# Kernel tuning notes

Measured on AMD Instinct MI355X. Metric: run time of the kernel, lower is better.

Reference implementation:

```python
import jax, jax.numpy as jnp
import numpy as np

# NVFP4 e2m1 representable magnitudes and nearest-rounding decision boundaries
FP4_GRID = jnp.array([0.0, 0.5, 1.0, 1.5, 2.0, 3.0, 4.0, 6.0], dtype=jnp.float32)
FP4_BOUNDS = jnp.array([0.25, 0.75, 1.25, 1.75, 2.5, 3.5, 5.0], dtype=jnp.float32)
E4M3_MAX = 448.0
FP4_MAX = 6.0
BLOCK = 16  # NVFP4 block size along K


def round_fp4(x):
    """Round to nearest FP4 (e2m1) representable value (saturating at +-6)."""
    idx = jnp.searchsorted(FP4_BOUNDS, jnp.abs(x))
    return jnp.sign(x) * FP4_GRID[idx]


def cast_e4m3(x):
    """Saturating cast through float8_e4m3fn and back to fp32."""
    return jnp.clip(x, -E4M3_MAX, E4M3_MAX).astype(jnp.float8_e4m3fn).astype(jnp.float32)


def setup_inputs() -> dict:
    key = jax.random.key(0)
    kx, kw, kb = jax.random.split(key, 3)
    M, N, K = 32, 8192, 8192
    x = jax.random.normal(kx, (M, K), dtype=jnp.float32)
    w = jax.random.normal(kw, (N, K), dtype=jnp.float32)
    bias = jax.random.normal(kb, (N,), dtype=jnp.float32)

    # raw global scales: amax / (448 * 6)  (== 1 / fp4_global_scale)
    weight_scale_2 = jnp.max(jnp.abs(w)) / (E4M3_MAX * FP4_MAX)
    input_scale = jnp.max(jnp.abs(x)) / (E4M3_MAX * FP4_MAX)

    # offline NVFP4 quantization of the weight (as done in __init__)
    wb = w.reshape(N, K // BLOCK, BLOCK)
    sf = jnp.max(jnp.abs(wb), axis=-1) / FP4_MAX              # [N, K//16] per-block scale
    weight_scale = cast_e4m3(sf / weight_scale_2)             # fp8 block scales (values)
    dscale = weight_scale[..., None] * weight_scale_2         # per-element dequant scale
    safe = jnp.where(dscale > 0, dscale, 1.0)
    w_fp4 = jnp.where(dscale > 0, round_fp4(wb / safe), 0.0).reshape(N, K)

    return {
        "x": x,
        "weight_fp4": w_fp4,
        "bias": bias,
        "input_scale": input_scale.reshape(1),
        "weight_scale": weight_scale,
        "weight_scale_2": weight_scale_2.reshape(1),
    }


def reference(x, weight_fp4, bias, input_scale, weight_scale, weight_scale_2):
    N, K = weight_fp4.shape
    M = x.shape[0]
    # --- weight dequant: fp4 value * fp8 block scale * global scale ---
    w_dq = (weight_fp4.reshape(N, K // BLOCK, BLOCK)
            * weight_scale[..., None] * weight_scale_2).reshape(N, K)
    # --- dynamic NVFP4 fake-quant of the activation ---
    xb = x.reshape(M, K // BLOCK, BLOCK)
    sf = cast_e4m3(jnp.max(jnp.abs(xb), axis=-1) / FP4_MAX / input_scale)  # [M, K//16]
    scale = sf[..., None] * input_scale                                    # per-element scale
    safe = jnp.where(scale > 0, scale, 1.0)
    x_dq = jnp.where(scale > 0, round_fp4(xb / safe) * scale, 0.0).reshape(M, K)
    # --- linear ---
    return x_dq @ w_dq.T + bias
```

## Files before the change

### kernel.cpp

```cpp
#include <hip/hip_runtime.h>

typedef float f32x4 __attribute__((ext_vector_type(4)));
typedef short s16x8 __attribute__((ext_vector_type(8)));

#define M_DIM 32
#define N_DIM 8192
#define K_DIM 8192
#define NBLK (K_DIM / 16)
#define KSPLIT 4
#define WSTEPS 16
#define SCL_LD 129

__device__ inline unsigned short f2bf(float f) {
    unsigned int u = __float_as_uint(f);
    u = (u + 0x7FFFu + ((u >> 16) & 1u)) >> 16;
    return (unsigned short)u;
}

__device__ inline float round_fp4(float x) {
    float a = fabsf(x);
    float g;
    if (a > 2.5f)        g = (a > 5.0f) ? 6.0f : ((a > 3.5f) ? 4.0f : 3.0f);
    else if (a > 1.25f)  g = (a > 1.75f) ? 2.0f : 1.5f;
    else                 g = (a > 0.75f) ? 1.0f : ((a > 0.25f) ? 0.5f : 0.0f);
    return copysignf(g, x);
}

__device__ inline float cast_e4m3(float v) {
    v = fminf(v, 448.0f);
    if (v < 0.015625f) {
        return rintf(v * 512.0f) * (1.0f / 512.0f);
    }
    int e; float m = frexpf(v, &e);
    return ldexpf(rintf(m * 16.0f) * 0.0625f, e);
}

__global__ void prep_kernel(const float* __restrict__ x,
                            const float* __restrict__ input_scale,
                            const float* __restrict__ bias,
                            unsigned short* __restrict__ xpack,
                            float* __restrict__ out) {
    if (blockIdx.x >= 64) {
        int i = (blockIdx.x - 64) * blockDim.x + threadIdx.x;
        f32x4 b = *(const f32x4*)(bias + ((i * 4) & (N_DIM - 1)));
        *(f32x4*)(out + (size_t)i * 4) = b;
        return;
    }
    int tid = blockIdx.x * blockDim.x + threadIdx.x;
    int m = tid >> 9;
    int b = tid & 511;
    const float is = input_scale[0];

    const float* xp = x + (size_t)m * K_DIM + b * 16;
    f32x4 l0 = *(const f32x4*)(xp);
    f32x4 l1 = *(const f32x4*)(xp + 4);
    f32x4 l2 = *(const f32x4*)(xp + 8);
    f32x4 l3 = *(const f32x4*)(xp + 12);
    float v[16];
    #pragma unroll
    for (int i = 0; i < 4; ++i) { v[i]=l0[i]; v[4+i]=l1[i]; v[8+i]=l2[i]; v[12+i]=l3[i]; }

    float amax = 0.f;
    #pragma unroll
    for (int i = 0; i < 16; ++i) amax = fmaxf(amax, fabsf(v[i]));

    float sf = cast_e4m3(amax / 6.0f / is);
    float scale = sf * is;

    int kstep = b >> 1;
    int t = m >> 4;
    int mrow = m & 15;
    unsigned short* base = xpack + (size_t)kstep * 1024 + t * 512;
    #pragma unroll
    for (int i = 0; i < 16; ++i) {
        float q = 0.f;
        if (scale > 0.f) q = round_fp4(v[i] / scale) * scale;
        int g = ((b & 1) << 1) + (i >> 3);
        int lane = g * 16 + mrow;
        int j = i & 7;
        base[lane * 8 + j] = f2bf(q);
    }
}

__global__ __launch_bounds__(256, 8) void gemm_kernel(
    const float* __restrict__ W,
    const float* __restrict__ wscale,
    const float* __restrict__ ws2p,
    const unsigned short* __restrict__ xpack,
    float* __restrict__ out)
{
    __shared__ float shm[16 * SCL_LD];

    const int bid   = blockIdx.x;
    const int xcd   = bid & 7;
    const int local = bid >> 3;
    const int ntile = xcd * 64 + (local >> 2);
    const int kb    = local & 3;

    const int wave = threadIdx.x >> 6;
    const int lane = threadIdx.x & 63;
    const int lrow = lane & 15;
    const int lgrp = lane >> 4;
    const int n0 = ntile * 16;
    const float ws2 = ws2p[0];

    {
        int t = threadIdx.x;
        int row = t >> 4;
        int c0 = (t & 15) * 8;
        const float* s = wscale + (size_t)(n0 + row) * NBLK + kb * 128 + c0;
        #pragma unroll
        for (int j = 0; j < 8; ++j)
            shm[row * SCL_LD + c0 + j] = s[j] * ws2;
    }
    __syncthreads();

    const int kofs = kb * 2048 + wave * 512;
    const float* wcur = W + (size_t)(n0 + lrow) * K_DIM + kofs + lgrp * 8;
    const unsigned short* xcur = xpack + (size_t)(kofs >> 5) * 1024 + lane * 8;
    const float* sbase = shm + lrow * SCL_LD + wave * 32 + (lgrp >> 1);

    f32x4 acc0 = {0,0,0,0}, acc1 = {0,0,0,0};

    f32x4 a0 = *(const f32x4*)(wcur);
    f32x4 a1 = *(const f32x4*)(wcur + 4);
    s16x8 b0 = *(const s16x8*)(xcur);
    s16x8 b1 = *(const s16x8*)(xcur + 512);

    #pragma unroll
    for (int s = 0; s < WSTEPS; ++s) {
        f32x4 na0, na1; s16x8 nb0, nb1;
        if (s + 1 < WSTEPS) {
            na0 = *(const f32x4*)(wcur + 32);
            na1 = *(const f32x4*)(wcur + 36);
            nb0 = *(const s16x8*)(xcur + 1024);
            nb1 = *(const s16x8*)(xcur + 1536);
        }
        float sc = sbase[s * 2];
        s16x8 af;
        #pragma unroll
        for (int j = 0; j < 4; ++j) {
            af[j]     = (short)f2bf(a0[j] * sc);
            af[4 + j] = (short)f2bf(a1[j] * sc);
        }
        acc0 = __builtin_amdgcn_mfma_f32_16x16x32_bf16(af, b0, acc0, 0, 0, 0);
        acc1 = __builtin_amdgcn_mfma_f32_16x16x32_bf16(af, b1, acc1, 0, 0, 0);
        a0 = na0; a1 = na1; b0 = nb0; b1 = nb1;
        wcur += 32;
        xcur += 1024;
    }

    __syncthreads();
    float* red = shm;
    #pragma unroll
    for (int r = 0; r < 4; ++r) {
        red[wave * 512 + lane * 8 + r]     = acc0[r];
        red[wave * 512 + lane * 8 + 4 + r] = acc1[r];
    }
    __syncthreads();

    #pragma unroll
    for (int h = 0; h < 2; ++h) {
        int j = threadIdx.x + h * 256;
        float v = red[j] + red[512 + j] + red[1024 + j] + red[1536 + j];
        int l = j >> 3, t = (j >> 2) & 1, r = j & 3;
        int m = t * 16 + (l & 15);
        int n = n0 + ((l >> 4) << 2) + r;
        atomicAdd(out + (size_t)m * N_DIM + n, v);
    }
}

extern "C" void kernel_launch(void* const* d_in, const int* in_sizes, int n_in,
                              void* d_out, int out_size, void* d_ws, size_t ws_size,
                              hipStream_t stream) {
    const float* x           = (const float*)d_in[0];
    const float* weight_fp4  = (const float*)d_in[1];
    const float* bias        = (const float*)d_in[2];
    const float* input_scale = (const float*)d_in[3];
    const float* wscale      = (const float*)d_in[4];
    const float* ws2         = (const float*)d_in[5];
    float* out = (float*)d_out;
    unsigned short* xpack = (unsigned short*)d_ws;

    prep_kernel<<<320, 256, 0, stream>>>(x, input_scale, bias, xpack, out);
    gemm_kernel<<<2048, 256, 0, stream>>>(weight_fp4, wscale, ws2, xpack, out);
}
```

Measured before the change: 67.22 us.

## Switch GEMM to 32x32x16 MFMA with 32-row N tiles and 8-way K split

Replaces the pair of 16x16x32 bf16 MFMAs per step with two 32x32x16 MFMAs. Each block now covers 32 weight rows and all 32 activation rows, and K is split 8 ways instead of 4, keeping the block count at 2048. The activation pack layout in the prep kernel is changed to match, with vectorized stores. The aim is to issue fewer MFMA and load instructions per FLOP and to reuse each weight row across the full M dimension. In exchange the kernel does more shared-memory reduction work and more atomics per output element because of the deeper K split.

```diff
diff --git a/kernel.cpp b/kernel.cpp
--- a/kernel.cpp
+++ b/kernel.cpp
@@ -1,15 +1,16 @@
 #include <hip/hip_runtime.h>
 
 typedef float f32x4 __attribute__((ext_vector_type(4)));
-typedef short s16x8 __attribute__((ext_vector_type(8)));
+typedef short s16x4 __attribute__((ext_vector_type(4)));
+typedef float f32x16 __attribute__((ext_vector_type(16)));
 
 #define M_DIM 32
 #define N_DIM 8192
 #define K_DIM 8192
 #define NBLK (K_DIM / 16)
-#define KSPLIT 4
-#define WSTEPS 16
-#define SCL_LD 129
+#define KSPLIT 8
+#define SSTEPS 8
+#define SCL_LD 66
 
 __device__ inline unsigned short f2bf(float f) {
     unsigned int u = __float_as_uint(f);
@@ -67,18 +68,21 @@
     float sf = cast_e4m3(amax / 6.0f / is);
     float scale = sf * is;
 
-    int kstep = b >> 1;
-    int t = m >> 4;
-    int mrow = m & 15;
-    unsigned short* base = xpack + (size_t)kstep * 1024 + t * 512;
-    #pragma unroll
-    for (int i = 0; i < 16; ++i) {
-        float q = 0.f;
-        if (scale > 0.f) q = round_fp4(v[i] / scale) * scale;
-        int g = ((b & 1) << 1) + (i >> 3);
-        int lane = g * 16 + mrow;
-        int j = i & 7;
-        base[lane * 8 + j] = f2bf(q);
+    int ss = b >> 1;
+    int t  = b & 1;
+    unsigned short* base = xpack + ((size_t)ss * 4 + t * 2) * 256 + m * 8;
+    #pragma unroll
+    for (int h = 0; h < 2; ++h) {
+        unsigned short tmp[8];
+        #pragma unroll
+        for (int j = 0; j < 8; ++j) {
+            float q = 0.f;
+            int i = h * 8 + j;
+            if (scale > 0.f) q = round_fp4(v[i] / scale) * scale;
+            tmp[j] = f2bf(q);
+        }
+        *(s16x4*)(base + h * 256)     = *(s16x4*)(tmp);
+        *(s16x4*)(base + h * 256 + 4) = *(s16x4*)(tmp + 4);
     }
 }
 
@@ -89,63 +93,84 @@
     const unsigned short* __restrict__ xpack,
     float* __restrict__ out)
 {
-    __shared__ float shm[16 * SCL_LD];
+    __shared__ float shm[4096];
 
     const int bid   = blockIdx.x;
     const int xcd   = bid & 7;
     const int local = bid >> 3;
-    const int ntile = xcd * 64 + (local >> 2);
-    const int kb    = local & 3;
+    const int ntile = xcd * 32 + (local >> 3);
+    const int kb    = local & 7;
 
     const int wave = threadIdx.x >> 6;
     const int lane = threadIdx.x & 63;
-    const int lrow = lane & 15;
-    const int lgrp = lane >> 4;
-    const int n0 = ntile * 16;
+    const int lrow = lane & 31;
+    const int half = lane >> 5;
+    const int n0 = ntile * 32;
     const float ws2 = ws2p[0];
 
     {
         int t = threadIdx.x;
-        int row = t >> 4;
-        int c0 = (t & 15) * 8;
-        const float* s = wscale + (size_t)(n0 + row) * NBLK + kb * 128 + c0;
+        int row = t >> 3;
+        int c0 = (t & 7) * 8;
+        const float* s = wscale + (size_t)(n0 + row) * NBLK + kb * 64 + c0;
         #pragma unroll
         for (int j = 0; j < 8; ++j)
             shm[row * SCL_LD + c0 + j] = s[j] * ws2;
     }
     __syncthreads();
 
-    const int kofs = kb * 2048 + wave * 512;
-    const float* wcur = W + (size_t)(n0 + lrow) * K_DIM + kofs + lgrp * 8;
-    const unsigned short* xcur = xpack + (size_t)(kofs >> 5) * 1024 + lane * 8;
-    const float* sbase = shm + lrow * SCL_LD + wave * 32 + (lgrp >> 1);
-
-    f32x4 acc0 = {0,0,0,0}, acc1 = {0,0,0,0};
-
-    f32x4 a0 = *(const f32x4*)(wcur);
-    f32x4 a1 = *(const f32x4*)(wcur + 4);
-    s16x8 b0 = *(const s16x8*)(xcur);
-    s16x8 b1 = *(const s16x8*)(xcur + 512);
-
-    #pragma unroll
-    for (int s = 0; s < WSTEPS; ++s) {
-        f32x4 na0, na1; s16x8 nb0, nb1;
-        if (s + 1 < WSTEPS) {
-            na0 = *(const f32x4*)(wcur + 32);
-            na1 = *(const f32x4*)(wcur + 36);
-            nb0 = *(const s16x8*)(xcur + 1024);
-            nb1 = *(const s16x8*)(xcur + 1536);
-        }
-        float sc = sbase[s * 2];
-        s16x8 af;
+    const int kofs = kb * 1024 + wave * 256;
+    const float* wcur = W + (size_t)(n0 + lrow) * K_DIM + kofs + half * 8;
+    const unsigned short* xcur = xpack + ((size_t)(kofs >> 5) * 4 + half) * 256 + lrow * 8;
+    const float* sbase = shm + lrow * SCL_LD + (kofs >> 4) - (size_t)(n0 + 0) * 0 - kb * 64 + 0;
+    const float* scur = shm + lrow * SCL_LD + wave * 16;
+
+    f32x16 acc = {};
+
+    f32x4 a00 = *(const f32x4*)(wcur);
+    f32x4 a01 = *(const f32x4*)(wcur + 4);
+    f32x4 a10 = *(const f32x4*)(wcur + 16);
+    f32x4 a11 = *(const f32x4*)(wcur + 20);
+    s16x4 b00 = *(const s16x4*)(xcur);
+    s16x4 b01 = *(const s16x4*)(xcur + 4);
+    s16x4 b10 = *(const s16x4*)(xcur + 512);
+    s16x4 b11 = *(const s16x4*)(xcur + 516);
+
+    #pragma unroll
+    for (int s = 0; s < SSTEPS; ++s) {
+        f32x4 na00, na01, na10, na11; s16x4 nb00, nb01, nb10, nb11;
+        if (s + 1 < SSTEPS) {
+            na00 = *(const f32x4*)(wcur + 32);
+            na01 = *(const f32x4*)(wcur + 36);
+            na10 = *(const f32x4*)(wcur + 48);
+            na11 = *(const f32x4*)(wcur + 52);
+            nb00 = *(const s16x4*)(xcur + 1024);
+            nb01 = *(const s16x4*)(xcur + 1028);
+            nb10 = *(const s16x4*)(xcur + 1536);
+            nb11 = *(const s16x4*)(xcur + 1540);
+        }
+        float sc0 = scur[2 * s];
+        float sc1 = scur[2 * s + 1];
+        typedef short s16x8 __attribute__((ext_vector_type(8)));
+        s16x8 af, bf;
         #pragma unroll
         for (int j = 0; j < 4; ++j) {
-            af[j]     = (short)f2bf(a0[j] * sc);
-            af[4 + j] = (short)f2bf(a1[j] * sc);
-        }
-        acc0 = __builtin_amdgcn_mfma_f32_16x16x32_bf16(af, b0, acc0, 0, 0, 0);
-        acc1 = __builtin_amdgcn_mfma_f32_16x16x32_bf16(af, b1, acc1, 0, 0, 0);
-        a0 = na0; a1 = na1; b0 = nb0; b1 = nb1;
+            af[j]     = (short)f2bf(a00[j] * sc0);
+            af[4 + j] = (short)f2bf(a01[j] * sc0);
+            bf[j]     = b00[j];
+            bf[4 + j] = b01[j];
+        }
+        acc = __builtin_amdgcn_mfma_f32_32x32x16_bf16(af, bf, acc, 0, 0, 0);
+        #pragma unroll
+        for (int j = 0; j < 4; ++j) {
+            af[j]     = (short)f2bf(a10[j] * sc1);
+            af[4 + j] = (short)f2bf(a11[j] * sc1);
+            bf[j]     = b10[j];
+            bf[4 + j] = b11[j];
+        }
+        acc = __builtin_amdgcn_mfma_f32_32x32x16_bf16(af, bf, acc, 0, 0, 0);
+        a00 = na00; a01 = na01; a10 = na10; a11 = na11;
+        b00 = nb00; b01 = nb01; b10 = nb10; b11 = nb11;
         wcur += 32;
         xcur += 1024;
     }
@@ -153,19 +178,18 @@
     __syncthreads();
     float* red = shm;
     #pragma unroll
-    for (int r = 0; r < 4; ++r) {
-        red[wave * 512 + lane * 8 + r]     = acc0[r];
-        red[wave * 512 + lane * 8 + 4 + r] = acc1[r];
+    for (int r = 0; r < 16; ++r) {
+        int row = (r & 3) + 8 * (r >> 2) + 4 * half;
+        red[wave * 1024 + row * 32 + lrow] = acc[r];
     }
     __syncthreads();
 
     #pragma unroll
-    for (int h = 0; h < 2; ++h) {
+    for (int h = 0; h < 4; ++h) {
         int j = threadIdx.x + h * 256;
-        float v = red[j] + red[512 + j] + red[1024 + j] + red[1536 + j];
-        int l = j >> 3, t = (j >> 2) & 1, r = j & 3;
-        int m = t * 16 + (l & 15);
-        int n = n0 + ((l >> 4) << 2) + r;
+        float v = red[j] + red[1024 + j] + red[2048 + j] + red[3072 + j];
+        int m = j & 31;
+        int n = n0 + (j >> 5);
         atomicAdd(out + (size_t)m * N_DIM + n, v);
     }
 }
```

Result: slower. 93.41 us (+39.0%).

## Widen GEMM tiles to 32 rows of N with 8-way K split

Applied to the files above, without the earlier changes.

Each block now covers 32 weight rows instead of 16 and splits K eight ways instead of four, so each wave issues four MFMAs per step and reuses every activation fragment for two weight row groups. The explicit software prefetch of the next step's loads is removed in favour of issuing all loads at the top of each unrolled step. The reduction layout is changed so the atomic adds go to consecutive m indices. The grid size stays 2048 blocks, so more atomics per output element are traded for better reuse of the activation loads and more memory requests in flight per wave.

```diff
diff --git a/kernel.cpp b/kernel.cpp
--- a/kernel.cpp
+++ b/kernel.cpp
@@ -7,9 +7,8 @@
 #define N_DIM 8192
 #define K_DIM 8192
 #define NBLK (K_DIM / 16)
-#define KSPLIT 4
-#define WSTEPS 16
-#define SCL_LD 129
+#define SSTEPS 8
+#define SCL_LD 65
 
 __device__ inline unsigned short f2bf(float f) {
     unsigned int u = __float_as_uint(f);
@@ -89,83 +88,84 @@
     const unsigned short* __restrict__ xpack,
     float* __restrict__ out)
 {
-    __shared__ float shm[16 * SCL_LD];
+    __shared__ float shm[4096];
 
     const int bid   = blockIdx.x;
     const int xcd   = bid & 7;
     const int local = bid >> 3;
-    const int ntile = xcd * 64 + (local >> 2);
-    const int kb    = local & 3;
+    const int ntile = xcd * 32 + (local >> 3);
+    const int kb    = local & 7;
 
     const int wave = threadIdx.x >> 6;
     const int lane = threadIdx.x & 63;
     const int lrow = lane & 15;
     const int lgrp = lane >> 4;
-    const int n0 = ntile * 16;
+    const int n0 = ntile * 32;
     const float ws2 = ws2p[0];
 
     {
         int t = threadIdx.x;
-        int row = t >> 4;
-        int c0 = (t & 15) * 8;
-        const float* s = wscale + (size_t)(n0 + row) * NBLK + kb * 128 + c0;
+        int row = t >> 3;
+        int c0 = (t & 7) * 8;
+        const float* s = wscale + (size_t)(n0 + row) * NBLK + kb * 64 + c0;
         #pragma unroll
         for (int j = 0; j < 8; ++j)
             shm[row * SCL_LD + c0 + j] = s[j] * ws2;
     }
     __syncthreads();
 
-    const int kofs = kb * 2048 + wave * 512;
-    const float* wcur = W + (size_t)(n0 + lrow) * K_DIM + kofs + lgrp * 8;
+    const int kofs = kb * 1024 + wave * 256;
+    const float* wcur0 = W + (size_t)(n0 + lrow) * K_DIM + kofs + lgrp * 8;
+    const float* wcur1 = wcur0 + (size_t)16 * K_DIM;
     const unsigned short* xcur = xpack + (size_t)(kofs >> 5) * 1024 + lane * 8;
-    const float* sbase = shm + lrow * SCL_LD + wave * 32 + (lgrp >> 1);
+    const float* scur0 = shm + lrow * SCL_LD + wave * 16 + (lgrp >> 1);
+    const float* scur1 = scur0 + 16 * SCL_LD;
 
-    f32x4 acc0 = {0,0,0,0}, acc1 = {0,0,0,0};
-
-    f32x4 a0 = *(const f32x4*)(wcur);
-    f32x4 a1 = *(const f32x4*)(wcur + 4);
-    s16x8 b0 = *(const s16x8*)(xcur);
-    s16x8 b1 = *(const s16x8*)(xcur + 512);
+    f32x4 acc00 = {0,0,0,0}, acc01 = {0,0,0,0};
+    f32x4 acc10 = {0,0,0,0}, acc11 = {0,0,0,0};
 
     #pragma unroll
-    for (int s = 0; s < WSTEPS; ++s) {
-        f32x4 na0, na1; s16x8 nb0, nb1;
-        if (s + 1 < WSTEPS) {
-            na0 = *(const f32x4*)(wcur + 32);
-            na1 = *(const f32x4*)(wcur + 36);
-            nb0 = *(const s16x8*)(xcur + 1024);
-            nb1 = *(const s16x8*)(xcur + 1536);
-        }
-        float sc = sbase[s * 2];
-        s16x8 af;
+    for (int s = 0; s < SSTEPS; ++s) {
+        f32x4 a00 = *(const f32x4*)(wcur0 + s * 32);
+        f32x4 a01 = *(const f32x4*)(wcur0 + s * 32 + 4);
+        f32x4 a10 = *(const f32x4*)(wcur1 + s * 32);
+        f32x4 a11 = *(const f32x4*)(wcur1 + s * 32 + 4);
+        s16x8 b0 = *(const s16x8*)(xcur + (size_t)s * 1024);
+        s16x8 b1 = *(const s16x8*)(xcur + (size_t)s * 1024 + 512);
+        float sc0 = scur0[2 * s];
+        float sc1 = scur1[2 * s];
+        s16x8 af0, af1;
         #pragma unroll
         for (int j = 0; j < 4; ++j) {
-            af[j]     = (short)f2bf(a0[j] * sc);
-            af[4 + j] = (short)f2bf(a1[j] * sc);
+            af0[j]     = (short)f2bf(a00[j] * sc0);
+            af0[4 + j] = (short)f2bf(a01[j] * sc0);
+            af1[j]     = (short)f2bf(a10[j] * sc1);
+            af1[4 + j] = (short)f2bf(a11[j] * sc1);
         }
-        acc0 = __builtin_amdgcn_mfma_f32_16x16x32_bf16(af, b0, acc0, 0, 0, 0);
-        acc1 = __builtin_amdgcn_mfma_f32_16x16x32_bf16(af, b1, acc1, 0, 0, 0);
-        a0 = na0; a1 = na1; b0 = nb0; b1 = nb1;
-        wcur += 32;
-        xcur += 1024;
+        acc00 = __builtin_amdgcn_mfma_f32_16x16x32_bf16(af0, b0, acc00, 0, 0, 0);
+        acc01 = __builtin_amdgcn_mfma_f32_16x16x32_bf16(af0, b1, acc01, 0, 0, 0);
+        acc10 = __builtin_amdgcn_mfma_f32_16x16x32_bf16(af1, b0, acc10, 0, 0, 0);
+        acc11 = __builtin_amdgcn_mfma_f32_16x16x32_bf16(af1, b1, acc11, 0, 0, 0);
     }
 
     __syncthreads();
     float* red = shm;
     #pragma unroll
     for (int r = 0; r < 4; ++r) {
-        red[wave * 512 + lane * 8 + r]     = acc0[r];
-        red[wave * 512 + lane * 8 + 4 + r] = acc1[r];
+        int nl = lgrp * 4 + r;
+        red[wave * 1024 + nl * 32 + lrow]              = acc00[r];
+        red[wave * 1024 + nl * 32 + 16 + lrow]         = acc01[r];
+        red[wave * 1024 + (16 + nl) * 32 + lrow]       = acc10[r];
+        red[wave * 1024 + (16 + nl) * 32 + 16 + lrow]  = acc11[r];
     }
     __syncthreads();
 
     #pragma unroll
-    for (int h = 0; h < 2; ++h) {
+    for (int h = 0; h < 4; ++h) {
         int j = threadIdx.x + h * 256;
-        float v = red[j] + red[512 + j] + red[1024 + j] + red[1536 + j];
-        int l = j >> 3, t = (j >> 2) & 1, r = j & 3;
-        int m = t * 16 + (l & 15);
-        int n = n0 + ((l >> 4) << 2) + r;
+        float v = red[j] + red[1024 + j] + red[2048 + j] + red[3072 + j];
+        int m = j & 31;
+        int n = n0 + (j >> 5);
         atomicAdd(out + (size_t)m * N_DIM + n, v);
     }
 }
```

After: 89.14 us. +32.6%, slower.

## Share activation tile across four N-waves via async LDS load, split K 32-way

Applied to the files above, without the earlier changes.

Each block now covers 64 output columns (one 16-column slice per wave) over a 256-wide K chunk, split 32 ways along K. The packed activation tile for that chunk is staged once into LDS with global_load_lds and reused by all four waves, instead of every wave reading activations from global memory. Per-wave results go straight out through atomics, which removes the cross-wave LDS reduction. The cost is twice as many blocks and far more atomicAdd traffic to the output (a 32-way K split instead of 4), along with shorter per-block loops that have less prefetch depth.

```diff
diff --git a/kernel.cpp b/kernel.cpp
--- a/kernel.cpp
+++ b/kernel.cpp
@@ -7,9 +7,7 @@
 #define N_DIM 8192
 #define K_DIM 8192
 #define NBLK (K_DIM / 16)
-#define KSPLIT 4
-#define WSTEPS 16
-#define SCL_LD 129
+#define SSTEPS 8
 
 __device__ inline unsigned short f2bf(float f) {
     unsigned int u = __float_as_uint(f);
@@ -33,6 +31,11 @@
     }
     int e; float m = frexpf(v, &e);
     return ldexpf(rintf(m * 16.0f) * 0.0625f, e);
+}
+
+__device__ __forceinline__ void async_copy16(const void* g, void* l) {
+    __builtin_amdgcn_global_load_lds((const __attribute__((address_space(1))) void*)g,
+                                     (__attribute__((address_space(3))) void*)l, 16, 0, 0);
 }
 
 __global__ void prep_kernel(const float* __restrict__ x,
@@ -89,54 +92,59 @@
     const unsigned short* __restrict__ xpack,
     float* __restrict__ out)
 {
-    __shared__ float shm[16 * SCL_LD];
+    __shared__ __align__(16) unsigned char xq[16384];
+    __shared__ float sc_lds[1024];
 
     const int bid   = blockIdx.x;
     const int xcd   = bid & 7;
     const int local = bid >> 3;
-    const int ntile = xcd * 64 + (local >> 2);
-    const int kb    = local & 3;
+    const int ntile = xcd * 16 + (local >> 5);
+    const int kb    = local & 31;
 
     const int wave = threadIdx.x >> 6;
     const int lane = threadIdx.x & 63;
     const int lrow = lane & 15;
     const int lgrp = lane >> 4;
-    const int n0 = ntile * 16;
+    const int n0 = ntile * 64;
     const float ws2 = ws2p[0];
 
     {
+        const unsigned short* xsrc = xpack + (size_t)kb * 8192;
+        #pragma unroll
+        for (int i = 0; i < 4; ++i) {
+            int c = i * 4 + wave;
+            async_copy16(xsrc + c * 512 + lane * 8, xq + c * 1024);
+        }
+    }
+    {
         int t = threadIdx.x;
-        int row = t >> 4;
-        int c0 = (t & 15) * 8;
-        const float* s = wscale + (size_t)(n0 + row) * NBLK + kb * 128 + c0;
+        int row = t >> 2;
+        int c0 = (t & 3) * 4;
+        f32x4 s4 = *(const f32x4*)(wscale + (size_t)(n0 + row) * NBLK + kb * 16 + c0);
         #pragma unroll
-        for (int j = 0; j < 8; ++j)
-            shm[row * SCL_LD + c0 + j] = s[j] * ws2;
+        for (int j = 0; j < 4; ++j) s4[j] *= ws2;
+        *(f32x4*)(sc_lds + row * 16 + c0) = s4;
     }
     __syncthreads();
 
-    const int kofs = kb * 2048 + wave * 512;
-    const float* wcur = W + (size_t)(n0 + lrow) * K_DIM + kofs + lgrp * 8;
-    const unsigned short* xcur = xpack + (size_t)(kofs >> 5) * 1024 + lane * 8;
-    const float* sbase = shm + lrow * SCL_LD + wave * 32 + (lgrp >> 1);
+    const float* wcur = W + (size_t)(n0 + wave * 16 + lrow) * K_DIM + kb * 256 + lgrp * 8;
+    const float* scur = sc_lds + (wave * 16 + lrow) * 16 + (lgrp >> 1);
 
     f32x4 acc0 = {0,0,0,0}, acc1 = {0,0,0,0};
 
     f32x4 a0 = *(const f32x4*)(wcur);
     f32x4 a1 = *(const f32x4*)(wcur + 4);
-    s16x8 b0 = *(const s16x8*)(xcur);
-    s16x8 b1 = *(const s16x8*)(xcur + 512);
 
     #pragma unroll
-    for (int s = 0; s < WSTEPS; ++s) {
-        f32x4 na0, na1; s16x8 nb0, nb1;
-        if (s + 1 < WSTEPS) {
+    for (int s = 0; s < SSTEPS; ++s) {
+        f32x4 na0, na1;
+        if (s + 1 < SSTEPS) {
             na0 = *(const f32x4*)(wcur + 32);
             na1 = *(const f32x4*)(wcur + 36);
-            nb0 = *(const s16x8*)(xcur + 1024);
-            nb1 = *(const s16x8*)(xcur + 1536);
         }
-        float sc = sbase[s * 2];
+        s16x8 b0 = *(const s16x8*)(xq + s * 2048 + lane * 16);
+        s16x8 b1 = *(const s16x8*)(xq + s * 2048 + 1024 + lane * 16);
+        float sc = scur[2 * s];
         s16x8 af;
         #pragma unroll
         for (int j = 0; j < 4; ++j) {
@@ -145,28 +153,15 @@
         }
         acc0 = __builtin_amdgcn_mfma_f32_16x16x32_bf16(af, b0, acc0, 0, 0, 0);
         acc1 = __builtin_amdgcn_mfma_f32_16x16x32_bf16(af, b1, acc1, 0, 0, 0);
-        a0 = na0; a1 = na1; b0 = nb0; b1 = nb1;
+        a0 = na0; a1 = na1;
         wcur += 32;
-        xcur += 1024;
     }
 
-    __syncthreads();
-    float* red = shm;
     #pragma unroll
     for (int r = 0; r < 4; ++r) {
-        red[wave * 512 + lane * 8 + r]     = acc0[r];
-        red[wave * 512 + lane * 8 + 4 + r] = acc1[r];
-    }
-    __syncthreads();
-
-    #pragma unroll
-    for (int h = 0; h < 2; ++h) {
-        int j = threadIdx.x + h * 256;
-        float v = red[j] + red[512 + j] + red[1024 + j] + red[1536 + j];
-        int l = j >> 3, t = (j >> 2) & 1, r = j & 3;
-        int m = t * 16 + (l & 15);
-        int n = n0 + ((l >> 4) << 2) + r;
-        atomicAdd(out + (size_t)m * N_DIM + n, v);
+        int n = n0 + wave * 16 + lgrp * 4 + r;
+        atomicAdd(out + (size_t)lrow * N_DIM + n,        acc0[r]);
+        atomicAdd(out + (size_t)(16 + lrow) * N_DIM + n, acc1[r]);
     }
 }
 
@@ -183,5 +178,5 @@
     unsigned short* xpack = (unsigned short*)d_ws;
 
     prep_kernel<<<320, 256, 0, stream>>>(x, input_scale, bias, xpack, out);
-    gemm_kernel<<<2048, 256, 0, stream>>>(weight_fp4, wscale, ws2, xpack, out);
+    gemm_kernel<<<4096, 256, 0, stream>>>(weight_fp4, wscale, ws2, xpack, out);
 }
```

Result: slower. 133.4 us (+98.4%).
